# Optimization experiments

Hardware: AMD Instinct MI355X
Metric: run time of the kernel (lower is better)

## Reference

```python
import jax, jax.numpy as jnp
import numpy as np

DIM = 2048
NUM_HEADS = 16
NUM_KV_HEADS = 4
HEAD_DIM = DIM // NUM_HEADS  # 128
GROUP = NUM_HEADS // NUM_KV_HEADS  # queries per kv head
B, N = 2, 2048


def setup_inputs() -> dict:
    key = jax.random.key(0)
    ks = jax.random.split(key, 5)
    s = 1.0 / np.sqrt(DIM)
    return {
        "x": jax.random.normal(ks[0], (B, N, DIM), dtype=jnp.float32),
        "Wq": jax.random.normal(ks[1], (DIM, DIM), dtype=jnp.float32) * s,
        "Wk": jax.random.normal(ks[2], (DIM, NUM_KV_HEADS * HEAD_DIM), dtype=jnp.float32) * s,
        "Wv": jax.random.normal(ks[3], (DIM, NUM_KV_HEADS * HEAD_DIM), dtype=jnp.float32) * s,
        "Wo": jax.random.normal(ks[4], (DIM, DIM), dtype=jnp.float32) * s,
    }


def reference(x, Wq, Wk, Wv, Wo):
    Bc, Nc, C = x.shape
    scale = HEAD_DIM ** -0.5
    # projections -> [B, H, N, D] / [B, Hkv, N, D]
    q = (x @ Wq).reshape(Bc, Nc, NUM_HEADS, HEAD_DIM).transpose(0, 2, 1, 3)
    k = (x @ Wk).reshape(Bc, Nc, NUM_KV_HEADS, HEAD_DIM).transpose(0, 2, 1, 3)
    v = (x @ Wv).reshape(Bc, Nc, NUM_KV_HEADS, HEAD_DIM).transpose(0, 2, 1, 3)
    # repeat_interleave over head dim: kv head i serves query heads [i*G, (i+1)*G)
    k = jnp.repeat(k, GROUP, axis=1)  # [B, H, N, D]
    v = jnp.repeat(v, GROUP, axis=1)
    attn = jnp.einsum("bhqd,bhkd->bhqk", q, k) * scale
    attn = jax.nn.softmax(attn, axis=-1)
    out = jnp.einsum("bhqk,bhkd->bhqd", attn, v)  # [B, H, N, D]
    out = out.transpose(0, 2, 1, 3).reshape(Bc, Nc, C)
    return out @ Wo
```

## Files before the change

kernel.cpp:

```cpp
#include <hip/hip_runtime.h>
#include <hip/hip_bf16.h>
#include <cstdint>
#include <cstddef>

typedef __bf16 bf16;
typedef __attribute__((ext_vector_type(8))) __bf16 bf16x8;
typedef __attribute__((ext_vector_type(4))) float f32x4;
typedef __attribute__((ext_vector_type(16))) float f32x16;
typedef unsigned int u32;
typedef __attribute__((ext_vector_type(2))) unsigned int u32x2;

#define DEVINL __device__ __forceinline__

DEVINL void gload16(const void* g, void* l) {
  __builtin_amdgcn_global_load_lds(
      (const __attribute__((address_space(1))) void*)g,
      (__attribute__((address_space(3))) void*)l, 16, 0, 0);
}

DEVINL f32x4 mfma16(bf16x8 a, bf16x8 b, f32x4 c) {
  return __builtin_amdgcn_mfma_f32_16x16x32_bf16(a, b, c, 0, 0, 0);
}
DEVINL f32x16 mfma32(bf16x8 a, bf16x8 b, f32x16 c) {
  return __builtin_amdgcn_mfma_f32_32x32x16_bf16(a, b, c, 0, 0, 0);
}
DEVINL u32 cvtpk(float lo, float hi) {
  u32 r;
  asm("v_cvt_pk_bf16_f32 %0, %1, %2" : "=v"(r) : "v"(lo), "v"(hi));
  return r;
}
DEVINL void plswap(u32& a, u32& b) {
  asm("v_permlane32_swap_b32 %0, %1" : "+v"(a), "+v"(b));
}

__global__ __launch_bounds__(256) void cast_x_kernel(const float* __restrict__ x,
                                                     bf16* __restrict__ o, int n8) {
  int i = blockIdx.x * 256 + threadIdx.x;
  if (i >= n8) return;
  f32x4 a = ((const f32x4*)x)[2 * i];
  f32x4 b = ((const f32x4*)x)[2 * i + 1];
  bf16x8 v;
#pragma unroll
  for (int k = 0; k < 4; ++k) { v[k] = (bf16)a[k]; v[4 + k] = (bf16)b[k]; }
  ((bf16x8*)o)[i] = v;
}

__global__ __launch_bounds__(256) void transpose_cast_kernel(const float* __restrict__ src,
                                                             bf16* __restrict__ dst,
                                                             int K, int N) {
  __shared__ float tile[64][65];
  int nt = N >> 6;
  int n0 = (blockIdx.x % nt) << 6;
  int k0 = (blockIdx.x / nt) << 6;
  int c = threadIdx.x & 63, rb = threadIdx.x >> 6;
#pragma unroll
  for (int rr = 0; rr < 16; ++rr) {
    int row = rr * 4 + rb;
    tile[row][c] = src[(size_t)(k0 + row) * N + n0 + c];
  }
  __syncthreads();
#pragma unroll
  for (int rr = 0; rr < 16; ++rr) {
    int nrow = rr * 4 + rb;
    dst[(size_t)(n0 + nrow) * K + k0 + c] = (bf16)tile[c][nrow];
  }
}

template <int EPI>
__global__ __launch_bounds__(256) void gemm_bt_kernel(const bf16* __restrict__ A,
                                                      const bf16* __restrict__ BT,
                                                      float* __restrict__ Cout,
                                                      int Mtiles,
                                                      bf16* __restrict__ qb,
                                                      bf16* __restrict__ kb_,
                                                      bf16* __restrict__ vtb) {
  __shared__ __align__(16) unsigned char smem[32768];
  const int t = threadIdx.x, w = t >> 6, lane = t & 63;
  const int l4 = lane >> 4, l16 = lane & 15;
  const int bm = blockIdx.x % Mtiles, bn = blockIdx.x / Mtiles;
  const int wm = w >> 1, wn = w & 1;

  const char* aP[2];
  const char* bP[2];
#pragma unroll
  for (int p = 0; p < 2; ++p) {
    int g = p * 256 + t;
    aP[p] = (const char*)A + (size_t)(bm * 128 + (g >> 2)) * 4096 + (g & 3) * 16;
    bP[p] = (const char*)BT + (size_t)(bn * 128 + (g >> 2)) * 4096 + (g & 3) * 16;
  }
  const unsigned ldsW = w * 1024;

  auto STAGE = [&](unsigned buf, int k0) {
    gload16(aP[0] + k0, smem + buf * 16384 + ldsW);
    gload16(aP[1] + k0, smem + buf * 16384 + 4096 + ldsW);
    gload16(bP[0] + k0, smem + buf * 16384 + 8192 + ldsW);
    gload16(bP[1] + k0, smem + buf * 16384 + 12288 + ldsW);
  };

  const f32x4 fz = {0.f, 0.f, 0.f, 0.f};
  f32x4 acc[4][4];
#pragma unroll
  for (int i = 0; i < 4; ++i)
#pragma unroll
    for (int j = 0; j < 4; ++j) acc[i][j] = fz;

  const int arow = 64 * wm + l16, brow = 64 * wn + l16, kbyte = 16 * l4;

  STAGE(0, 0);
  __syncthreads();

#pragma unroll 2
  for (int tt = 0; tt < 64; ++tt) {
    const unsigned buf = tt & 1;
    if (tt < 63) STAGE(buf ^ 1u, (tt + 1) * 64);
    bf16x8 af[4], bfr[4];
#pragma unroll
    for (int i = 0; i < 4; ++i)
      af[i] = *(const bf16x8*)(smem + buf * 16384 + (arow + 16 * i) * 64 + kbyte);
#pragma unroll
    for (int j = 0; j < 4; ++j)
      bfr[j] = *(const bf16x8*)(smem + buf * 16384 + 8192 + (brow + 16 * j) * 64 + kbyte);
#pragma unroll
    for (int i = 0; i < 4; ++i)
#pragma unroll
      for (int j = 0; j < 4; ++j)
        acc[i][j] = mfma16(af[i], bfr[j], acc[i][j]);
    __syncthreads();
  }

  const int r0 = bm * 128 + 64 * wm + 4 * l4;
  if (EPI == 1) {
#pragma unroll
    for (int j = 0; j < 4; ++j) {
      int col = bn * 128 + 64 * wn + 16 * j + l16;
#pragma unroll
      for (int i = 0; i < 4; ++i)
#pragma unroll
        for (int r = 0; r < 4; ++r)
          Cout[(size_t)(r0 + 16 * i + r) * 2048 + col] = acc[i][j][r];
    }
  } else {
    const int bq = bm >> 4;
#pragma unroll
    for (int j = 0; j < 4; ++j) {
      int col = bn * 128 + 64 * wn + 16 * j + l16;
      if (bn < 16) {
        int hh = col >> 7, d = col & 127;
        bf16* dst = qb + (size_t)((bq * 16 + hh) * 2048) * 128 + d;
#pragma unroll
        for (int i = 0; i < 4; ++i)
#pragma unroll
          for (int r = 0; r < 4; ++r) {
            int n = (r0 + 16 * i + r) & 2047;
            dst[(size_t)n * 128] = (bf16)acc[i][j][r];
          }
      } else if (bn < 20) {
        int kv = (col >> 7) - 16, d = col & 127;
        bf16* dst = kb_ + (size_t)((bq * 4 + kv) * 2048) * 128 + d;
#pragma unroll
        for (int i = 0; i < 4; ++i)
#pragma unroll
          for (int r = 0; r < 4; ++r) {
            int n = (r0 + 16 * i + r) & 2047;
            dst[(size_t)n * 128] = (bf16)acc[i][j][r];
          }
      } else {
        int kv = (col >> 7) - 20, d = col & 127;
        bf16* dst = vtb + ((size_t)(bq * 4 + kv) * 128 + d) * 2048;
#pragma unroll
        for (int i = 0; i < 4; ++i)
#pragma unroll
          for (int r = 0; r < 4; ++r) {
            int n = (r0 + 16 * i + r) & 2047;
            dst[n] = (bf16)acc[i][j][r];
          }
      }
    }
  }
}

__global__ __launch_bounds__(256, 2) void attn_kernel(const bf16* __restrict__ Q,
                                                      const bf16* __restrict__ K,
                                                      const bf16* __restrict__ VT,
                                                      bf16* __restrict__ AO) {
  __shared__ __align__(16) unsigned char smem[65536];
  const int t = threadIdx.x, w = t >> 6, lane = t & 63;
  const int q = lane & 31, hi = lane >> 5;
  const int pair = blockIdx.x >> 4;
  const int q00 = (blockIdx.x & 15) * 128 + w * 32;
  const int b = pair >> 4, h = pair & 15, kvh = h >> 2;
  const float KS2 = 0.08838834764831845f * 1.4426950408889634f;

  bf16x8 qf[8];
  {
    const char* qbase = (const char*)Q +
        ((size_t)((b * 16 + h) * 2048 + q00 + q) * 128 + 8 * hi) * 2;
#pragma unroll
    for (int dk = 0; dk < 8; ++dk) qf[dk] = *(const bf16x8*)(qbase + dk * 32);
  }

  f32x16 acc[4];
#pragma unroll
  for (int dt = 0; dt < 4; ++dt)
#pragma unroll
    for (int r = 0; r < 16; ++r) acc[dt][r] = 0.0f;
  float mrun = -1e30f, lrun = 0.0f;

  const char* Kg = (const char*)K + (size_t)((b * 4 + kvh) * 2048) * 256;
  const char* Vg = (const char*)VT + (size_t)((b * 4 + kvh) * 128) * 4096;

  auto STAGE_K = [&](int itn) {
    const unsigned base = (unsigned)(itn & 1) * 16384u;
    const int kb = itn * 64;
#pragma unroll
    for (int p = 0; p < 4; ++p) {
      int g = p * 256 + t;
      int row = g >> 4, cb = (g & 15) * 16;
      gload16(Kg + (size_t)(kb + row) * 256 + (cb ^ ((row & 15) << 4)),
              smem + base + p * 4096 + w * 1024);
    }
  };
  auto STAGE_V = [&](int itn) {
    const unsigned base = 32768u + (unsigned)(itn & 1) * 16384u;
    const int kb = itn * 64;
#pragma unroll
    for (int p = 0; p < 4; ++p) {
      int g = p * 256 + t;
      int row = g >> 3, cb = (g & 7) * 16;
      gload16(Vg + (size_t)row * 4096 + kb * 2 + (cb ^ ((row & 7) << 4)),
              smem + base + p * 4096 + w * 1024);
    }
  };

  auto SMFMA = [&](int itn, f32x16& s0, f32x16& s1) {
    const unsigned base = (unsigned)(itn & 1) * 16384u;
    const unsigned swq = (q & 15) << 4;
#pragma unroll
    for (int r = 0; r < 16; ++r) { s0[r] = 0.0f; s1[r] = 0.0f; }
    __builtin_amdgcn_s_setprio(1);
#pragma unroll
    for (int dk = 0; dk < 8; ++dk) {
      const int cb = dk * 32 + 16 * hi;
      bf16x8 k0 = *(const bf16x8*)(smem + base + q * 256 + (cb ^ swq));
      bf16x8 k1 = *(const bf16x8*)(smem + base + (q + 32) * 256 + (cb ^ swq));
      s0 = mfma32(k0, qf[dk], s0);
      s1 = mfma32(k1, qf[dk], s1);
    }
    __builtin_amdgcn_s_setprio(0);
  };

  auto FINISH = [&](int itn, f32x16& s0, f32x16& s1) {
    float tm[16];
#pragma unroll
    for (int r = 0; r < 16; ++r) tm[r] = fmaxf(s0[r], s1[r]);
#pragma unroll
    for (int st = 8; st; st >>= 1)
#pragma unroll
      for (int r = 0; r < 8; ++r)
        if (r < st) tm[r] = fmaxf(tm[r], tm[r + st]);
    float mo = tm[0];
    mo = fmaxf(mo, __shfl_xor(mo, 32, 64));
    if (!__all((mo - mrun) * KS2 <= 8.0f)) {
      float mn = fmaxf(mrun, mo);
      float al = __builtin_amdgcn_exp2f((mrun - mn) * KS2);
      lrun *= al;
#pragma unroll
      for (int dt = 0; dt < 4; ++dt)
#pragma unroll
        for (int r = 0; r < 16; ++r) acc[dt][r] *= al;
      mrun = mn;
    }
    const float c0 = KS2 * mrun;
    float p0[16], p1[16];
#pragma unroll
    for (int r = 0; r < 16; ++r) {
      p0[r] = __builtin_amdgcn_exp2f(s0[r] * KS2 - c0);
      p1[r] = __builtin_amdgcn_exp2f(s1[r] * KS2 - c0);
    }
    float ts[16];
#pragma unroll
    for (int r = 0; r < 16; ++r) ts[r] = p0[r] + p1[r];
#pragma unroll
    for (int st = 8; st; st >>= 1)
#pragma unroll
      for (int r = 0; r < 8; ++r)
        if (r < st) ts[r] += ts[r + st];
    float rs = ts[0];
    rs += __shfl_xor(rs, 32, 64);
    lrun += rs;

    bf16x8 pa[4];
#pragma unroll
    for (int ks = 0; ks < 4; ++ks) {
      const int bs = (ks & 1) * 8;
      float* P = (ks >> 1) ? p1 : p0;
      u32 A0 = cvtpk(P[bs + 0], P[bs + 1]);
      u32 A1 = cvtpk(P[bs + 2], P[bs + 3]);
      u32 B0 = cvtpk(P[bs + 4], P[bs + 5]);
      u32 B1 = cvtpk(P[bs + 6], P[bs + 7]);
      plswap(A0, B0);
      plswap(A1, B1);
      union { u32 u[4]; bf16x8 v; } pu;
      pu.u[0] = A0; pu.u[1] = A1; pu.u[2] = B0; pu.u[3] = B1;
      pa[ks] = pu.v;
    }

    const unsigned vbase = 32768u + (unsigned)(itn & 1) * 16384u;
    __builtin_amdgcn_s_setprio(1);
#pragma unroll
    for (int ks = 0; ks < 4; ++ks) {
      const int kcol = ks * 32 + 16 * hi;
      const unsigned swd = (q & 7) << 4;
      bf16x8 va0 = *(const bf16x8*)(smem + vbase + (0 * 32 + q) * 128 + (kcol ^ swd));
      bf16x8 va1 = *(const bf16x8*)(smem + vbase + (1 * 32 + q) * 128 + (kcol ^ swd));
      bf16x8 va2 = *(const bf16x8*)(smem + vbase + (2 * 32 + q) * 128 + (kcol ^ swd));
      bf16x8 va3 = *(const bf16x8*)(smem + vbase + (3 * 32 + q) * 128 + (kcol ^ swd));
      acc[0] = mfma32(va0, pa[ks], acc[0]);
      acc[1] = mfma32(va1, pa[ks], acc[1]);
      acc[2] = mfma32(va2, pa[ks], acc[2]);
      acc[3] = mfma32(va3, pa[ks], acc[3]);
    }
    __builtin_amdgcn_s_setprio(0);
  };

  f32x16 sA0, sA1, sB0, sB1;
  STAGE_K(0);
  __syncthreads();

  STAGE_K(1);
  STAGE_V(0);
  SMFMA(0, sA0, sA1);
  __syncthreads();

#pragma unroll 1
  for (int i = 1; i < 31; i += 2) {
    STAGE_K(i + 1);
    STAGE_V(i);
    SMFMA(i, sB0, sB1);
    FINISH(i - 1, sA0, sA1);
    __syncthreads();
    STAGE_K(i + 2);
    STAGE_V(i + 1);
    SMFMA(i + 1, sA0, sA1);
    FINISH(i, sB0, sB1);
    __syncthreads();
  }

  STAGE_V(31);
  SMFMA(31, sB0, sB1);
  FINISH(30, sA0, sA1);
  __syncthreads();
  FINISH(31, sB0, sB1);

  const float inv = 1.0f / lrun;
  bf16* aorow = AO + (size_t)(b * 2048 + q00 + q) * 2048 + h * 128;
#pragma unroll
  for (int dt = 0; dt < 4; ++dt)
#pragma unroll
    for (int rq = 0; rq < 4; ++rq) {
      u32 w0 = cvtpk(acc[dt][rq * 4 + 0] * inv, acc[dt][rq * 4 + 1] * inv);
      u32 w1 = cvtpk(acc[dt][rq * 4 + 2] * inv, acc[dt][rq * 4 + 3] * inv);
      u32x2 pr; pr.x = w0; pr.y = w1;
      *(u32x2*)(aorow + dt * 32 + rq * 8 + 4 * hi) = pr;
    }
}

extern "C" void kernel_launch(void* const* d_in, const int* in_sizes, int n_in,
                              void* d_out, int out_size, void* d_ws, size_t ws_size,
                              hipStream_t stream) {
  const float* x = (const float*)d_in[0];
  const float* Wq = (const float*)d_in[1];
  const float* Wk = (const float*)d_in[2];
  const float* Wv = (const float*)d_in[3];
  const float* Wo = (const float*)d_in[4];

  char* ws = (char*)d_ws;
  bf16* xbf = (bf16*)(ws);
  bf16* WqkvT = (bf16*)(ws + 16777216);
  bf16* WoT = (bf16*)(ws + 29360128);
  bf16* Qbuf = (bf16*)(ws + 37748736);
  bf16* Kbuf = (bf16*)(ws + 54525952);
  bf16* VTbuf = (bf16*)(ws + 58720256);

  cast_x_kernel<<<4096, 256, 0, stream>>>(x, xbf, 1048576);
  transpose_cast_kernel<<<1024, 256, 0, stream>>>(Wq, WqkvT, 2048, 2048);
  transpose_cast_kernel<<<256, 256, 0, stream>>>(Wk, WqkvT + (size_t)2048 * 2048, 2048, 512);
  transpose_cast_kernel<<<256, 256, 0, stream>>>(Wv, WqkvT + (size_t)2560 * 2048, 2048, 512);
  transpose_cast_kernel<<<1024, 256, 0, stream>>>(Wo, WoT, 2048, 2048);

  gemm_bt_kernel<0><<<768, 256, 0, stream>>>(xbf, WqkvT, nullptr, 32, Qbuf, Kbuf, VTbuf);
  attn_kernel<<<512, 256, 0, stream>>>(Qbuf, Kbuf, VTbuf, xbf);
  gemm_bt_kernel<1><<<512, 256, 0, stream>>>(xbf, WoT, (float*)d_out, 32, nullptr, nullptr, nullptr);
}
```

Before: 211.5 us.

## Merge prep kernels, triple-buffer GEMM loads, and swizzle GEMM block order

Five cast/transpose launches are merged into a single prep kernel that dispatches on block index, which removes launch overhead and the gaps between kernels. The GEMM moves from a double-buffered LDS pipeline to a triple-buffered one, prefetching two k-steps ahead and using explicit vmcnt waits with raw barriers in place of __syncthreads. Block indices are also swizzled across groups of eight so neighbouring workgroups share A and B tiles in cache. LDS use per GEMM block grows to 48 KB, which may lower occupancy.

```diff
diff --git a/kernel.cpp b/kernel.cpp
--- a/kernel.cpp
+++ b/kernel.cpp
@@ -33,26 +33,38 @@
   asm("v_permlane32_swap_b32 %0, %1" : "+v"(a), "+v"(b));
 }
 
-__global__ __launch_bounds__(256) void cast_x_kernel(const float* __restrict__ x,
-                                                     bf16* __restrict__ o, int n8) {
-  int i = blockIdx.x * 256 + threadIdx.x;
-  if (i >= n8) return;
-  f32x4 a = ((const f32x4*)x)[2 * i];
-  f32x4 b = ((const f32x4*)x)[2 * i + 1];
-  bf16x8 v;
-#pragma unroll
-  for (int k = 0; k < 4; ++k) { v[k] = (bf16)a[k]; v[4 + k] = (bf16)b[k]; }
-  ((bf16x8*)o)[i] = v;
-}
-
-__global__ __launch_bounds__(256) void transpose_cast_kernel(const float* __restrict__ src,
-                                                             bf16* __restrict__ dst,
-                                                             int K, int N) {
+__global__ __launch_bounds__(256) void prep_kernel(const float* __restrict__ x,
+                                                   const float* __restrict__ Wq,
+                                                   const float* __restrict__ Wk,
+                                                   const float* __restrict__ Wv,
+                                                   const float* __restrict__ Wo,
+                                                   bf16* __restrict__ xbf,
+                                                   bf16* __restrict__ WqkvT,
+                                                   bf16* __restrict__ WoT) {
+  const int bid = blockIdx.x, t = threadIdx.x;
+  if (bid < 4096) {
+    int i = bid * 256 + t;
+    f32x4 a = ((const f32x4*)x)[2 * i];
+    f32x4 b2 = ((const f32x4*)x)[2 * i + 1];
+    bf16x8 v;
+#pragma unroll
+    for (int k = 0; k < 4; ++k) { v[k] = (bf16)a[k]; v[4 + k] = (bf16)b2[k]; }
+    ((bf16x8*)xbf)[i] = v;
+    return;
+  }
   __shared__ float tile[64][65];
+  const float* src;
+  bf16* dst;
+  int N, blk;
+  if (bid < 5120)      { src = Wq; dst = WqkvT;                        N = 2048; blk = bid - 4096; }
+  else if (bid < 5376) { src = Wk; dst = WqkvT + (size_t)2048 * 2048;  N = 512;  blk = bid - 5120; }
+  else if (bid < 5632) { src = Wv; dst = WqkvT + (size_t)2560 * 2048;  N = 512;  blk = bid - 5376; }
+  else                 { src = Wo; dst = WoT;                          N = 2048; blk = bid - 5632; }
+  const int K = 2048;
   int nt = N >> 6;
-  int n0 = (blockIdx.x % nt) << 6;
-  int k0 = (blockIdx.x / nt) << 6;
-  int c = threadIdx.x & 63, rb = threadIdx.x >> 6;
+  int n0 = (blk % nt) << 6;
+  int k0 = (blk / nt) << 6;
+  int c = t & 63, rb = t >> 6;
 #pragma unroll
   for (int rr = 0; rr < 16; ++rr) {
     int row = rr * 4 + rb;
@@ -74,10 +86,11 @@
                                                       bf16* __restrict__ qb,
                                                       bf16* __restrict__ kb_,
                                                       bf16* __restrict__ vtb) {
-  __shared__ __align__(16) unsigned char smem[32768];
+  __shared__ __align__(16) unsigned char smem[49152];
   const int t = threadIdx.x, w = t >> 6, lane = t & 63;
   const int l4 = lane >> 4, l16 = lane & 15;
-  const int bm = blockIdx.x % Mtiles, bn = blockIdx.x / Mtiles;
+  const int swz = (blockIdx.x & 7) * ((int)gridDim.x >> 3) + (blockIdx.x >> 3);
+  const int bm = swz % Mtiles, bn = swz / Mtiles;
   const int wm = w >> 1, wn = w & 1;
 
   const char* aP[2];
@@ -90,11 +103,11 @@
   }
   const unsigned ldsW = w * 1024;
 
-  auto STAGE = [&](unsigned buf, int k0) {
-    gload16(aP[0] + k0, smem + buf * 16384 + ldsW);
-    gload16(aP[1] + k0, smem + buf * 16384 + 4096 + ldsW);
-    gload16(bP[0] + k0, smem + buf * 16384 + 8192 + ldsW);
-    gload16(bP[1] + k0, smem + buf * 16384 + 12288 + ldsW);
+  auto STAGE = [&](unsigned off, int k0) {
+    gload16(aP[0] + k0, smem + off + ldsW);
+    gload16(aP[1] + k0, smem + off + 4096 + ldsW);
+    gload16(bP[0] + k0, smem + off + 8192 + ldsW);
+    gload16(bP[1] + k0, smem + off + 12288 + ldsW);
   };
 
   const f32x4 fz = {0.f, 0.f, 0.f, 0.f};
@@ -107,25 +120,34 @@
   const int arow = 64 * wm + l16, brow = 64 * wn + l16, kbyte = 16 * l4;
 
   STAGE(0, 0);
-  __syncthreads();
-
-#pragma unroll 2
+  STAGE(16384, 64);
+  asm volatile("s_waitcnt vmcnt(4)" ::: "memory");
+  __builtin_amdgcn_s_barrier();
+  __builtin_amdgcn_sched_barrier(0);
+
+  unsigned off0 = 0, off1 = 16384, off2 = 32768;
+#pragma unroll 1
   for (int tt = 0; tt < 64; ++tt) {
-    const unsigned buf = tt & 1;
-    if (tt < 63) STAGE(buf ^ 1u, (tt + 1) * 64);
+    if (tt < 62) STAGE(off2, (tt + 2) * 64);
     bf16x8 af[4], bfr[4];
 #pragma unroll
     for (int i = 0; i < 4; ++i)
-      af[i] = *(const bf16x8*)(smem + buf * 16384 + (arow + 16 * i) * 64 + kbyte);
+      af[i] = *(const bf16x8*)(smem + off0 + (arow + 16 * i) * 64 + kbyte);
 #pragma unroll
     for (int j = 0; j < 4; ++j)
-      bfr[j] = *(const bf16x8*)(smem + buf * 16384 + 8192 + (brow + 16 * j) * 64 + kbyte);
+      bfr[j] = *(const bf16x8*)(smem + off0 + 8192 + (brow + 16 * j) * 64 + kbyte);
 #pragma unroll
     for (int i = 0; i < 4; ++i)
 #pragma unroll
       for (int j = 0; j < 4; ++j)
         acc[i][j] = mfma16(af[i], bfr[j], acc[i][j]);
-    __syncthreads();
+    if (tt < 63) {
+      if (tt < 62) asm volatile("s_waitcnt vmcnt(4)" ::: "memory");
+      else         asm volatile("s_waitcnt vmcnt(0)" ::: "memory");
+      __builtin_amdgcn_s_barrier();
+      __builtin_amdgcn_sched_barrier(0);
+    }
+    unsigned tmp = off0; off0 = off1; off1 = off2; off2 = tmp;
   }
 
   const int r0 = bm * 128 + 64 * wm + 4 * l4;
@@ -382,12 +404,7 @@
   bf16* Kbuf = (bf16*)(ws + 54525952);
   bf16* VTbuf = (bf16*)(ws + 58720256);
 
-  cast_x_kernel<<<4096, 256, 0, stream>>>(x, xbf, 1048576);
-  transpose_cast_kernel<<<1024, 256, 0, stream>>>(Wq, WqkvT, 2048, 2048);
-  transpose_cast_kernel<<<256, 256, 0, stream>>>(Wk, WqkvT + (size_t)2048 * 2048, 2048, 512);
-  transpose_cast_kernel<<<256, 256, 0, stream>>>(Wv, WqkvT + (size_t)2560 * 2048, 2048, 512);
-  transpose_cast_kernel<<<1024, 256, 0, stream>>>(Wo, WoT, 2048, 2048);
-
+  prep_kernel<<<6656, 256, 0, stream>>>(x, Wq, Wk, Wv, Wo, xbf, WqkvT, WoT);
   gemm_bt_kernel<0><<<768, 256, 0, stream>>>(xbf, WqkvT, nullptr, 32, Qbuf, Kbuf, VTbuf);
   attn_kernel<<<512, 256, 0, stream>>>(Qbuf, Kbuf, VTbuf, xbf);
   gemm_bt_kernel<1><<<512, 256, 0, stream>>>(xbf, WoT, (float*)d_out, 32, nullptr, nullptr, nullptr);
```

Measured after the change: 213.2 us. About the same (+0.8%).
